# Kernel optimization log

Measured on AMD Instinct MI355X. Metric: run time of the kernel, lower is better.

Reference implementation:

```python
import jax, jax.numpy as jnp
import numpy as np

N_NODES = 50000
N_EDGES = 800000
IN_F, HID, NCLS = 128, 64, 64
N_EXTRA = 2          # layer - 2
K_STEPS = 10
ALPHA = 0.1
BN_EPS = 1e-5


def setup_inputs() -> dict:
    key = jax.random.key(0)
    ks = jax.random.split(key, 20)
    d = {}
    d['x'] = jax.random.normal(ks[0], (N_NODES, IN_F), dtype=jnp.float32)
    d['edge_index'] = jax.random.randint(ks[1], (2, N_EDGES), 0, N_NODES, dtype=jnp.int64)
    s = 1.0 / np.sqrt(HID)
    d['W1'] = jax.random.normal(ks[2], (IN_F, HID), dtype=jnp.float32) / np.sqrt(IN_F)
    d['b1'] = jnp.zeros((HID,), jnp.float32)
    d['W2'] = jax.random.normal(ks[3], (HID, HID), dtype=jnp.float32) * s
    d['b2'] = jnp.zeros((HID,), jnp.float32)
    d['Wx'] = jax.random.normal(ks[4], (N_EXTRA, HID, HID), dtype=jnp.float32) * s
    d['bx'] = jnp.zeros((N_EXTRA, HID), jnp.float32)
    d['g1'] = jnp.ones((HID,), jnp.float32); d['be1'] = jnp.zeros((HID,), jnp.float32)
    d['g2'] = jnp.ones((HID,), jnp.float32); d['be2'] = jnp.zeros((HID,), jnp.float32)
    d['g3'] = jnp.ones((HID,), jnp.float32); d['be3'] = jnp.zeros((HID,), jnp.float32)
    d['Wfc'] = jax.random.normal(ks[5], (HID, NCLS), dtype=jnp.float32) * s
    d['bfc'] = jnp.zeros((NCLS,), jnp.float32)
    return d


def _gcn_norm(edge_index, n):
    # add self-loops, symmetric D^-1/2 (A+I) D^-1/2 normalization (PyG GCNConv default)
    loop = jnp.arange(n, dtype=edge_index.dtype)
    src = jnp.concatenate([edge_index[0], loop])
    dst = jnp.concatenate([edge_index[1], loop])
    deg = jax.ops.segment_sum(jnp.ones(src.shape[0], jnp.float32), dst, num_segments=n)
    dinv = jnp.where(deg > 0, jax.lax.rsqrt(deg), 0.0)
    return src, dst, dinv[src] * dinv[dst]


def _propagate(x, src, dst, w, n):
    # gather-scale-scatter: out[dst] += w * x[src]
    return jax.ops.segment_sum(x[src] * w[:, None], dst, num_segments=n)


def _bn(x, g, b):
    # BatchNorm1d in training mode: batch statistics over the node dim
    m = jnp.mean(x, axis=0)
    v = jnp.var(x, axis=0)
    return g * (x - m) * jax.lax.rsqrt(v + BN_EPS) + b


def reference(x, edge_index, W1, b1, W2, b2, Wx, bx, g1, be1, g2, be2, g3, be3, Wfc, bfc):
    n = x.shape[0]
    src, dst, w = _gcn_norm(edge_index, n)
    h = _propagate(x @ W1, src, dst, w, n) + b1
    h = jax.nn.relu(_bn(h, g1, be1))
    h = _propagate(h @ W2, src, dst, w, n) + b2
    h = jax.nn.relu(_bn(h, g2, be2))
    for i in range(Wx.shape[0]):
        h = _propagate(h @ Wx[i], src, dst, w, n) + bx[i]
        h = jax.nn.relu(_bn(h, g3, be3))
    # APPNP: K power-iteration steps with teleport back to h0
    h0 = h
    for _ in range(K_STEPS):
        h = (1.0 - ALPHA) * _propagate(h, src, dst, w, n) + ALPHA * h0
    out = h @ Wfc + bfc
    return jax.nn.log_softmax(out, axis=1)
```

## Files before the change

### kernel.cpp

```cpp
#include <hip/hip_runtime.h>
#include <hip/hip_fp16.h>
#include <cstdint>
#include <cstddef>

#define NN 50000
#define NE 800000
#define HID 64
#define INF_ 128
#define BN_EPS 1e-5f
#define NGRP (NN / 8)
#define NG16 (NN / 16)
#define SCAN_B 196
#define NSLICE 32
#define NBKT 16

typedef float floatx2 __attribute__((ext_vector_type(2)));

__device__ __forceinline__ float4 h8_to_f4(float2 raw) {
    union { float f; __half2 h; } ua, ub;
    ua.f = raw.x; ub.f = raw.y;
    float2 fa = __half22float2(ua.h), fb = __half22float2(ub.h);
    return make_float4(fa.x, fa.y, fb.x, fb.y);
}
__device__ __forceinline__ float2 f4_to_h8(float4 v) {
    union { float f; __half2 h; } ua, ub;
    ua.h = __float22half2_rn(make_float2(v.x, v.y));
    ub.h = __float22half2_rn(make_float2(v.z, v.w));
    return make_float2(ua.f, ub.f);
}
struct f8 { float v[8]; };
__device__ __forceinline__ f8 h16_to_f8(float4 raw) {
    f8 r;
    union { float f; __half2 h; } u;
    float2 a;
    u.f = raw.x; a = __half22float2(u.h); r.v[0] = a.x; r.v[1] = a.y;
    u.f = raw.y; a = __half22float2(u.h); r.v[2] = a.x; r.v[3] = a.y;
    u.f = raw.z; a = __half22float2(u.h); r.v[4] = a.x; r.v[5] = a.y;
    u.f = raw.w; a = __half22float2(u.h); r.v[6] = a.x; r.v[7] = a.y;
    return r;
}
__device__ __forceinline__ float4 f8_to_h16(const f8& s) {
    union { float f; __half2 h; } u;
    float4 o;
    u.h = __float22half2_rn(make_float2(s.v[0], s.v[1])); o.x = u.f;
    u.h = __float22half2_rn(make_float2(s.v[2], s.v[3])); o.y = u.f;
    u.h = __float22half2_rn(make_float2(s.v[4], s.v[5])); o.z = u.f;
    u.h = __float22half2_rn(make_float2(s.v[6], s.v[7])); o.w = u.f;
    return o;
}

__device__ __forceinline__ void fp8x8_to_f(unsigned lo, unsigned hi, float out[8]) {
    floatx2 a = __builtin_amdgcn_cvt_pk_f32_fp8((int)lo, false);
    floatx2 b = __builtin_amdgcn_cvt_pk_f32_fp8((int)lo, true);
    floatx2 c = __builtin_amdgcn_cvt_pk_f32_fp8((int)hi, false);
    floatx2 d = __builtin_amdgcn_cvt_pk_f32_fp8((int)hi, true);
    out[0] = a[0]; out[1] = a[1]; out[2] = b[0]; out[3] = b[1];
    out[4] = c[0]; out[5] = c[1]; out[6] = d[0]; out[7] = d[1];
}
__device__ __forceinline__ void fp8x16_to_f(uint4 r, float out[16]) {
    fp8x8_to_f(r.x, r.y, out);
    fp8x8_to_f(r.z, r.w, out + 8);
}
__device__ __forceinline__ uint2 f_to_fp8x8(const float v[8]) {
    int w0 = __builtin_amdgcn_cvt_pk_fp8_f32(v[0], v[1], 0, false);
    w0 = __builtin_amdgcn_cvt_pk_fp8_f32(v[2], v[3], w0, true);
    int w1 = __builtin_amdgcn_cvt_pk_fp8_f32(v[4], v[5], 0, false);
    w1 = __builtin_amdgcn_cvt_pk_fp8_f32(v[6], v[7], w1, true);
    uint2 o; o.x = (unsigned)w0; o.y = (unsigned)w1;
    return o;
}
__device__ __forceinline__ uint4 f_to_fp8x16(const float v[16]) {
    uint2 a = f_to_fp8x8(v), b = f_to_fp8x8(v + 8);
    uint4 o; o.x = a.x; o.y = a.y; o.z = b.x; o.w = b.y;
    return o;
}


__global__ void count_k(const int* __restrict__ dst, int* __restrict__ cnt) {
    int e = blockIdx.x * blockDim.x + threadIdx.x;
    if (e < NE) atomicAdd(&cnt[dst[e]], 1);
}

__global__ void dinv_k(const int* __restrict__ cnt, float* __restrict__ dinv) {
    int n = blockIdx.x * blockDim.x + threadIdx.x;
    if (n < NN) dinv[n] = rsqrtf((float)(cnt[n] + 1));
}

__global__ void scan1_k(const int* __restrict__ cnt, int* __restrict__ offs,
                        int* __restrict__ bsum) {
    __shared__ int sh[256];
    int t = threadIdx.x, i = blockIdx.x * 256 + t;
    int v = (i < NN) ? ((cnt[i] + 7) & ~7) : 0;
    sh[t] = v;
    __syncthreads();
    for (int d = 1; d < 256; d <<= 1) {
        int u = (t >= d) ? sh[t - d] : 0;
        __syncthreads();
        sh[t] += u;
        __syncthreads();
    }
    if (i < NN) offs[i] = sh[t] - v;
    if (t == 255) bsum[blockIdx.x] = sh[255];
}

__global__ void scan2_k(const int* __restrict__ bsum, int* __restrict__ bpre,
                        int* __restrict__ offs) {
    __shared__ int sh[256];
    int t = threadIdx.x;
    int v = (t < SCAN_B) ? bsum[t] : 0;
    sh[t] = v;
    __syncthreads();
    for (int d = 1; d < 256; d <<= 1) {
        int u = (t >= d) ? sh[t - d] : 0;
        __syncthreads();
        sh[t] += u;
        __syncthreads();
    }
    bpre[t] = sh[t] - v;
    if (t == 255) offs[NN] = sh[255];
}

__global__ void scan3_k(int* __restrict__ offs, const int* __restrict__ bpre) {
    int i = blockIdx.x * blockDim.x + threadIdx.x;
    if (i < NN) offs[i] += bpre[i >> 8];
}

__global__ void pad_k(const int* __restrict__ cnt, const int* __restrict__ offs,
                      int2* __restrict__ edge2) {
    int n = blockIdx.x * blockDim.x + threadIdx.x;
    if (n >= NN) return;
    int e = offs[n] + cnt[n], e1 = offs[n + 1];
    for (; e < e1; ++e) edge2[e] = make_int2(0, 0);
}

__global__ void scatter_k(const int* __restrict__ src, const int* __restrict__ dst,
                          const int* __restrict__ offs, int* __restrict__ cursor,
                          const float* __restrict__ dinv,
                          int2* __restrict__ edge2) {
    int e = blockIdx.x * blockDim.x + threadIdx.x;
    if (e < NE) {
        int s = src[e], d = dst[e];
        int pos = offs[d] + atomicAdd(&cursor[d], 1);
        edge2[pos] = make_int2(s, __float_as_int(dinv[s] * dinv[d]));
    }
}

__global__ void hist_k(const int* __restrict__ cnt, int* __restrict__ hist) {
    __shared__ int lh[NBKT];
    int t = threadIdx.x;
    if (t < NBKT) lh[t] = 0;
    __syncthreads();
    int n = blockIdx.x * 256 + t;
    if (n < NN) {
        int c = (cnt[n] + 7) >> 3;
        if (c > NBKT - 1) c = NBKT - 1;
        atomicAdd(&lh[c], 1);
    }
    __syncthreads();
    if (t < NBKT && lh[t]) atomicAdd(&hist[t], lh[t]);
}

__global__ void scan16_k(const int* __restrict__ hist, int* __restrict__ bcur) {
    if (threadIdx.x == 0) {
        int s = 0;
        for (int i = 0; i < NBKT; ++i) { bcur[i] = s; s += hist[i]; }
    }
}

__global__ void perm_k(const int* __restrict__ cnt, int* __restrict__ bcur,
                       int* __restrict__ perm) {
    __shared__ int lh[NBKT], lbase[NBKT];
    int t = threadIdx.x;
    if (t < NBKT) lh[t] = 0;
    __syncthreads();
    int n = blockIdx.x * 256 + t;
    int c = 0, r = 0;
    if (n < NN) {
        c = (cnt[n] + 7) >> 3;
        if (c > NBKT - 1) c = NBKT - 1;
        r = atomicAdd(&lh[c], 1);
    }
    __syncthreads();
    if (t < NBKT) lbase[t] = lh[t] ? atomicAdd(&bcur[t], lh[t]) : 0;
    __syncthreads();
    if (n < NN) perm[lbase[c] + r] = n;
}

template <int K, bool HIN>
__global__ __launch_bounds__(256, 2) void mm_k(const void* __restrict__ Xv,
                                               const float* __restrict__ W,
                                               float2* __restrict__ Y) {
    constexpr int RS = K + 4;
    __shared__ float Xs[64 * RS];
    __shared__ float Ws[K * 64];
    const int t = threadIdx.x;
    const int n0 = blockIdx.x * 64;

    {
        const float4* Wg = (const float4*)W;
        for (int g2 = t; g2 < K * 16; g2 += 256) {
            int row = g2 >> 4, c4 = g2 & 15;
            *(float4*)&Ws[row * 64 + c4 * 4] = Wg[g2];
        }
    }
    if (HIN) {
        const float4* Xg = (const float4*)Xv;
        for (int g2 = t; g2 < 64 * (K / 8); g2 += 256) {
            int row = g2 / (K / 8), c8 = g2 % (K / 8);
            int rr = n0 + row; if (rr >= NN) rr = NN - 1;
            f8 v = h16_to_f8(Xg[(size_t)rr * (K / 8) + c8]);
            float* dp = &Xs[row * RS + c8 * 8];
#pragma unroll
            for (int j = 0; j < 8; ++j) dp[j] = v.v[j];
        }
    } else {
        const float4* Xg = (const float4*)Xv;
        for (int g2 = t; g2 < 64 * (K / 4); g2 += 256) {
            int row = g2 / (K / 4), c4 = g2 % (K / 4);
            int rr = n0 + row; if (rr >= NN) rr = NN - 1;
            *(float4*)&Xs[row * RS + c4 * 4] = Xg[(size_t)rr * (K / 4) + c4];
        }
    }
    __syncthreads();

    const int r0 = (t >> 4) << 2;
    const int c0 = (t & 15) << 2;
    float acc[4][4];
#pragma unroll
    for (int j = 0; j < 4; ++j)
#pragma unroll
        for (int c = 0; c < 4; ++c) acc[j][c] = 0.f;

#pragma unroll 8
    for (int kq = 0; kq < K / 4; ++kq) {
        float4 xv[4];
#pragma unroll
        for (int j = 0; j < 4; ++j)
            xv[j] = *(const float4*)&Xs[(r0 + j) * RS + kq * 4];
        float4 wv[4];
#pragma unroll
        for (int i = 0; i < 4; ++i)
            wv[i] = *(const float4*)&Ws[(kq * 4 + i) * 64 + c0];
#pragma unroll
        for (int j = 0; j < 4; ++j) {
            acc[j][0] = fmaf(xv[j].x, wv[0].x, acc[j][0]);
            acc[j][1] = fmaf(xv[j].x, wv[0].y, acc[j][1]);
            acc[j][2] = fmaf(xv[j].x, wv[0].z, acc[j][2]);
            acc[j][3] = fmaf(xv[j].x, wv[0].w, acc[j][3]);
            acc[j][0] = fmaf(xv[j].y, wv[1].x, acc[j][0]);
            acc[j][1] = fmaf(xv[j].y, wv[1].y, acc[j][1]);
            acc[j][2] = fmaf(xv[j].y, wv[1].z, acc[j][2]);
            acc[j][3] = fmaf(xv[j].y, wv[1].w, acc[j][3]);
            acc[j][0] = fmaf(xv[j].z, wv[2].x, acc[j][0]);
            acc[j][1] = fmaf(xv[j].z, wv[2].y, acc[j][1]);
            acc[j][2] = fmaf(xv[j].z, wv[2].z, acc[j][2]);
            acc[j][3] = fmaf(xv[j].z, wv[2].w, acc[j][3]);
            acc[j][0] = fmaf(xv[j].w, wv[3].x, acc[j][0]);
            acc[j][1] = fmaf(xv[j].w, wv[3].y, acc[j][1]);
            acc[j][2] = fmaf(xv[j].w, wv[3].z, acc[j][2]);
            acc[j][3] = fmaf(xv[j].w, wv[3].w, acc[j][3]);
        }
    }

#pragma unroll
    for (int j = 0; j < 4; ++j) {
        int rr = n0 + r0 + j;
        if (rr < NN)
            Y[(size_t)rr * 16 + (t & 15)] =
                f4_to_h8(make_float4(acc[j][0], acc[j][1], acc[j][2], acc[j][3]));
    }
}

__device__ __forceinline__ void prop_gather8(const float4* __restrict__ X4,
                                             const int2* __restrict__ E,
                                             int e0, int e1, int fl, int slotbase,
                                             float acc[8], float acc2[8]) {
    if (e0 >= e1) return;
    int2 d0 = E[e0 + fl];
    int srcs[8]; float ws[8];
#pragma unroll
    for (int i = 0; i < 8; ++i) {
        srcs[i] = __shfl(d0.x, slotbase + i, 64);
        ws[i]   = __shfl(__int_as_float(d0.y), slotbase + i, 64);
    }
    int2 d1;
    if (e0 + 8 < e1) d1 = E[e0 + 8 + fl];
    float4 rr[8];
#pragma unroll
    for (int i = 0; i < 8; ++i) rr[i] = X4[(size_t)srcs[i] * 8 + fl];

    for (int e = e0; e < e1; ) {
        int en = e + 8;
        float4 rn[8]; float wn[8];
        if (en < e1) {
            int sn[8];
#pragma unroll
            for (int i = 0; i < 8; ++i) {
                sn[i] = __shfl(d1.x, slotbase + i, 64);
                wn[i] = __shfl(__int_as_float(d1.y), slotbase + i, 64);
            }
            if (en + 8 < e1) d1 = E[en + 8 + fl];
#pragma unroll
            for (int i = 0; i < 8; ++i) rn[i] = X4[(size_t)sn[i] * 8 + fl];
        }
        __builtin_amdgcn_sched_barrier(0);
#pragma unroll
        for (int i = 0; i < 8; ++i) {
            f8 x = h16_to_f8(rr[i]);
            float* a = (i & 1) ? acc2 : acc;
#pragma unroll
            for (int j = 0; j < 8; ++j)
                a[j] = fmaf(ws[i], x.v[j], a[j]);
        }
        e = en;
        if (e < e1) {
#pragma unroll
            for (int i = 0; i < 8; ++i) { rr[i] = rn[i]; ws[i] = wn[i]; }
        }
    }
}

__global__ __launch_bounds__(256, 2) void prop_stats_k(
        const float4* __restrict__ X4, const int* __restrict__ offs,
        const int2* __restrict__ edge2, const float* __restrict__ dinv,
        const float* __restrict__ bias, const int* __restrict__ perm,
        float4* __restrict__ Y4, float* __restrict__ stats) {
    const int lane = threadIdx.x & 63;
    const int wave = threadIdx.x >> 6;
    const int slot = lane >> 3;
    const int fl = lane & 7;
    const int slotbase = lane & 56;
    const int wid = blockIdx.x * 4 + wave;
    const int nw = gridDim.x * 4;

    float bias8[8];
    {
        float4 b0 = ((const float4*)bias)[fl * 2];
        float4 b1 = ((const float4*)bias)[fl * 2 + 1];
        bias8[0] = b0.x; bias8[1] = b0.y; bias8[2] = b0.z; bias8[3] = b0.w;
        bias8[4] = b1.x; bias8[5] = b1.y; bias8[6] = b1.z; bias8[7] = b1.w;
    }

    float s1[8], s2[8];
#pragma unroll
    for (int j = 0; j < 8; ++j) { s1[j] = 0.f; s2[j] = 0.f; }

    for (int g = wid; g < NGRP; g += nw) {
        int n = perm[g * 8 + slot];
        float dn = dinv[n];
        float dd = dn * dn;
        f8 self = h16_to_f8(X4[(size_t)n * 8 + fl]);
        float acc[8], acc2[8];
#pragma unroll
        for (int j = 0; j < 8; ++j) { acc[j] = dd * self.v[j]; acc2[j] = 0.f; }
        int e0 = offs[n], e1 = offs[n + 1];
        prop_gather8(X4, edge2, e0, e1, fl, slotbase, acc, acc2);
        f8 o;
#pragma unroll
        for (int j = 0; j < 8; ++j) {
            float a = acc[j] + acc2[j] + bias8[j];
            o.v[j] = a;
            s1[j] += a;
            s2[j] = fmaf(a, a, s2[j]);
        }
        Y4[(size_t)n * 8 + fl] = f8_to_h16(o);
    }

#pragma unroll
    for (int m = 8; m <= 32; m <<= 1) {
#pragma unroll
        for (int j = 0; j < 8; ++j) {
            s1[j] += __shfl_xor(s1[j], m, 64);
            s2[j] += __shfl_xor(s2[j], m, 64);
        }
    }

    __shared__ float red[4][8][16];
    if (lane < 8) {
#pragma unroll
        for (int j = 0; j < 8; ++j) {
            red[wave][lane][j] = s1[j];
            red[wave][lane][8 + j] = s2[j];
        }
    }
    __syncthreads();
    int t = threadIdx.x;
    if (t < 128) {
        int j = t & 63;
        int isq = t >> 6;
        int fli = j >> 3, c = (j & 7) + isq * 8;
        float a = red[0][fli][c] + red[1][fli][c] + red[2][fli][c] + red[3][fli][c];
        atomicAdd(&stats[(blockIdx.x & (NSLICE - 1)) * 128 + isq * 64 + j], a);
    }
}

template <bool EMIT8>
__global__ __launch_bounds__(256) void bn_relu_k(
        const float4* __restrict__ Y4, const float* __restrict__ slices,
        const float* __restrict__ g, const float* __restrict__ be,
        float4* __restrict__ H4, uint2* __restrict__ X8) {
    __shared__ float fs[128];
    int t = threadIdx.x;
    if (t < 128) {
        float s = 0.f;
#pragma unroll
        for (int k = 0; k < NSLICE; ++k) s += slices[k * 128 + t];
        fs[t] = s;
    }
    __syncthreads();
    int i = blockIdx.x * blockDim.x + t;
    if (i >= NN * 8) return;
    int fg = i & 7;
    const float invN = 1.f / (float)NN;
    f8 y = h16_to_f8(Y4[i]);
    float4 gv0 = ((const float4*)g)[fg * 2];
    float4 gv1 = ((const float4*)g)[fg * 2 + 1];
    float4 bv0 = ((const float4*)be)[fg * 2];
    float4 bv1 = ((const float4*)be)[fg * 2 + 1];
    float gv[8] = { gv0.x, gv0.y, gv0.z, gv0.w, gv1.x, gv1.y, gv1.z, gv1.w };
    float bv[8] = { bv0.x, bv0.y, bv0.z, bv0.w, bv1.x, bv1.y, bv1.z, bv1.w };
    f8 o;
#pragma unroll
    for (int j = 0; j < 8; ++j) {
        float m = fs[fg * 8 + j] * invN;
        float v = fs[64 + fg * 8 + j] * invN - m * m;
        float val = fmaf(gv[j] * rsqrtf(v + BN_EPS), y.v[j] - m, bv[j]);
        o.v[j] = val > 0.f ? val : 0.f;
    }
    H4[i] = f8_to_h16(o);
    if (EMIT8) X8[i] = f_to_fp8x8(o.v);
}

template <bool OUT16>
__global__ __launch_bounds__(256, 2) void appnp8_k(
        const uint4* __restrict__ X8, const float4* __restrict__ H04,
        const int* __restrict__ offs, const int2* __restrict__ edge2,
        const float* __restrict__ dinv, const int* __restrict__ perm,
        uint4* __restrict__ Y8, float4* __restrict__ Y16) {
    const int lane = threadIdx.x & 63;
    const int wave = threadIdx.x >> 6;
    const int slot = lane >> 2;
    const int fl = lane & 3;
    const int quadbase = lane & 60;
    const int wid = blockIdx.x * 4 + wave;
    if (wid >= NG16) return;
    int n = perm[wid * 16 + slot];
    float dn = dinv[n];
    float dd = dn * dn;
    float acc[16];
    {
        float self[16];
        fp8x16_to_f(X8[(size_t)n * 4 + fl], self);
#pragma unroll
        for (int j = 0; j < 16; ++j) acc[j] = dd * self[j];
    }
    int e0 = offs[n], e1 = offs[n + 1];
    if (e0 < e1) {
        int4 d = ((const int4*)(edge2 + e0))[fl];
        int srcs[8]; float ws[8];
#pragma unroll
        for (int k = 0; k < 8; ++k) {
            int sl = quadbase + (k >> 1);
            srcs[k] = __shfl((k & 1) ? d.z : d.x, sl, 64);
            ws[k]   = __shfl(__int_as_float((k & 1) ? d.w : d.y), sl, 64);
        }
        int4 d1;
        if (e0 + 8 < e1) d1 = ((const int4*)(edge2 + e0 + 8))[fl];
        uint4 rr[8];
#pragma unroll
        for (int k = 0; k < 8; ++k) rr[k] = X8[(size_t)srcs[k] * 4 + fl];

        for (int e = e0; e < e1; ) {
            int en = e + 8;
            uint4 rn[8]; float wn[8];
            if (en < e1) {
                int sn[8];
#pragma unroll
                for (int k = 0; k < 8; ++k) {
                    int sl = quadbase + (k >> 1);
                    sn[k] = __shfl((k & 1) ? d1.z : d1.x, sl, 64);
                    wn[k] = __shfl(__int_as_float((k & 1) ? d1.w : d1.y), sl, 64);
                }
                if (en + 8 < e1) d1 = ((const int4*)(edge2 + en + 8))[fl];
#pragma unroll
                for (int k = 0; k < 8; ++k) rn[k] = X8[(size_t)sn[k] * 4 + fl];
            }
            __builtin_amdgcn_sched_barrier(0);
#pragma unroll
            for (int k = 0; k < 8; ++k) {
                float x[16];
                fp8x16_to_f(rr[k], x);
#pragma unroll
                for (int j = 0; j < 16; ++j)
                    acc[j] = fmaf(ws[k], x[j], acc[j]);
            }
            e = en;
            if (e < e1) {
#pragma unroll
                for (int k = 0; k < 8; ++k) { rr[k] = rn[k]; ws[k] = wn[k]; }
            }
        }
    }
    f8 ha = h16_to_f8(H04[(size_t)n * 8 + fl * 2]);
    f8 hb = h16_to_f8(H04[(size_t)n * 8 + fl * 2 + 1]);
    float o[16];
#pragma unroll
    for (int j = 0; j < 8; ++j) {
        o[j] = fmaf(0.9f, acc[j], 0.1f * ha.v[j]);
        o[8 + j] = fmaf(0.9f, acc[8 + j], 0.1f * hb.v[j]);
    }
    if (OUT16) {
        f8 lo, hi;
#pragma unroll
        for (int j = 0; j < 8; ++j) { lo.v[j] = o[j]; hi.v[j] = o[8 + j]; }
        Y16[(size_t)n * 8 + fl * 2] = f8_to_h16(lo);
        Y16[(size_t)n * 8 + fl * 2 + 1] = f8_to_h16(hi);
    } else {
        Y8[(size_t)n * 4 + fl] = f_to_fp8x16(o);
    }
}

__global__ __launch_bounds__(256) void final_k(const float2* __restrict__ H2,
                                               const float* __restrict__ Wfc,
                                               const float* __restrict__ bfc,
                                               float* __restrict__ out) {
    const int t = threadIdx.x;
    const int n0 = blockIdx.x * 64;
    const int r0 = (t >> 4) << 2;
    const int c0 = (t & 15) << 2;

    int r[4];
#pragma unroll
    for (int j = 0; j < 4; ++j) {
        int rr = n0 + r0 + j;
        r[j] = rr < NN ? rr : NN - 1;
    }
    const float2* Xr[4];
#pragma unroll
    for (int j = 0; j < 4; ++j) Xr[j] = H2 + (size_t)r[j] * 16;

    float4 bf = *(const float4*)(bfc + c0);
    float acc[4][4];
#pragma unroll
    for (int j = 0; j < 4; ++j) {
        acc[j][0] = bf.x; acc[j][1] = bf.y; acc[j][2] = bf.z; acc[j][3] = bf.w;
    }

#pragma unroll 4
    for (int kq = 0; kq < 16; ++kq) {
        float4 xv[4];
#pragma unroll
        for (int j = 0; j < 4; ++j) xv[j] = h8_to_f4(Xr[j][kq]);
        float4 wv[4];
#pragma unroll
        for (int i = 0; i < 4; ++i)
            wv[i] = *(const float4*)(Wfc + (size_t)(kq * 4 + i) * 64 + c0);
#pragma unroll
        for (int j = 0; j < 4; ++j) {
            acc[j][0] = fmaf(xv[j].x, wv[0].x, acc[j][0]);
            acc[j][1] = fmaf(xv[j].x, wv[0].y, acc[j][1]);
            acc[j][2] = fmaf(xv[j].x, wv[0].z, acc[j][2]);
            acc[j][3] = fmaf(xv[j].x, wv[0].w, acc[j][3]);
            acc[j][0] = fmaf(xv[j].y, wv[1].x, acc[j][0]);
            acc[j][1] = fmaf(xv[j].y, wv[1].y, acc[j][1]);
            acc[j][2] = fmaf(xv[j].y, wv[1].z, acc[j][2]);
            acc[j][3] = fmaf(xv[j].y, wv[1].w, acc[j][3]);
            acc[j][0] = fmaf(xv[j].z, wv[2].x, acc[j][0]);
            acc[j][1] = fmaf(xv[j].z, wv[2].y, acc[j][1]);
            acc[j][2] = fmaf(xv[j].z, wv[2].z, acc[j][2]);
            acc[j][3] = fmaf(xv[j].z, wv[2].w, acc[j][3]);
            acc[j][0] = fmaf(xv[j].w, wv[3].x, acc[j][0]);
            acc[j][1] = fmaf(xv[j].w, wv[3].y, acc[j][1]);
            acc[j][2] = fmaf(xv[j].w, wv[3].z, acc[j][2]);
            acc[j][3] = fmaf(xv[j].w, wv[3].w, acc[j][3]);
        }
    }

#pragma unroll
    for (int j = 0; j < 4; ++j) {
        float m = fmaxf(fmaxf(acc[j][0], acc[j][1]), fmaxf(acc[j][2], acc[j][3]));
#pragma unroll
        for (int d = 1; d <= 8; d <<= 1) m = fmaxf(m, __shfl_xor(m, d, 64));
        float s = expf(acc[j][0] - m) + expf(acc[j][1] - m) +
                  expf(acc[j][2] - m) + expf(acc[j][3] - m);
#pragma unroll
        for (int d = 1; d <= 8; d <<= 1) s += __shfl_xor(s, d, 64);
        float lse = m + logf(s);
        int rr = n0 + r0 + j;
        if (rr < NN)
            *(float4*)(out + (size_t)rr * 64 + c0) =
                make_float4(acc[j][0] - lse, acc[j][1] - lse,
                            acc[j][2] - lse, acc[j][3] - lse);
    }
}


static inline char* alignup(char* p, size_t a) {
    return (char*)(((uintptr_t)p + a - 1) & ~(uintptr_t)(a - 1));
}

extern "C" void kernel_launch(void* const* d_in, const int* in_sizes, int n_in,
                              void* d_out, int out_size, void* d_ws, size_t ws_size,
                              hipStream_t stream) {
    const float* x   = (const float*)d_in[0];
    const int*   ei  = (const int*)d_in[1];
    const float* W1  = (const float*)d_in[2];
    const float* b1  = (const float*)d_in[3];
    const float* W2  = (const float*)d_in[4];
    const float* b2  = (const float*)d_in[5];
    const float* Wx  = (const float*)d_in[6];
    const float* bx  = (const float*)d_in[7];
    const float* g1  = (const float*)d_in[8];
    const float* be1 = (const float*)d_in[9];
    const float* g2  = (const float*)d_in[10];
    const float* be2 = (const float*)d_in[11];
    const float* g3  = (const float*)d_in[12];
    const float* be3 = (const float*)d_in[13];
    const float* Wfc = (const float*)d_in[14];
    const float* bfc = (const float*)d_in[15];
    float* out = (float*)d_out;

    const int* srcA = ei;
    const int* dstA = ei + NE;

    char* p = (char*)d_ws;
    int*   deg    = (int*)p;   p += NN * 4;
    int*   cursor = (int*)p;   p += NN * 4;
    float* stats  = (float*)p; p += 4 * NSLICE * 128 * 4;
    int*   hist   = (int*)p;   p += NBKT * 4;
    size_t zbytes = (size_t)(p - (char*)d_ws);
    p = alignup(p, 512);
    int*   offs  = (int*)p;    p += (NN + 4) * 4;   p = alignup(p, 512);
    float* dinv  = (float*)p;  p += NN * 4;         p = alignup(p, 512);
    int*   bsum  = (int*)p;    p += 256 * 4;
    int*   bpre  = (int*)p;    p += 256 * 4;
    int*   bcur  = (int*)p;    p += NBKT * 4;       p = alignup(p, 512);
    int*   perm  = (int*)p;    p += NN * 4;         p = alignup(p, 512);
    int2*  edge2 = (int2*)p;   p += ((size_t)NE + 8 * NN + 256) * 8; p = alignup(p, 512);
    float4* tmpH = (float4*)p; p += (size_t)NN * 64 * 2; p = alignup(p, 512);
    float4* hbH  = (float4*)p; p += (size_t)NN * 64 * 2; p = alignup(p, 512);
    float4* apH  = (float4*)p; p += (size_t)NN * 64 * 2; p = alignup(p, 512);
    float4* pbH  = (float4*)p; p += (size_t)NN * 64 * 2; p = alignup(p, 512);
    uint4*  x8a  = (uint4*)p;  p += (size_t)NN * 64;     p = alignup(p, 512);
    uint4*  x8b  = (uint4*)p;  p += (size_t)NN * 64;

    hipMemsetAsync(d_ws, 0, zbytes, stream);

    count_k<<<(NE + 255) / 256, 256, 0, stream>>>(dstA, deg);
    dinv_k<<<(NN + 255) / 256, 256, 0, stream>>>(deg, dinv);
    hist_k<<<SCAN_B, 256, 0, stream>>>(deg, hist);
    scan16_k<<<1, 64, 0, stream>>>(hist, bcur);
    perm_k<<<SCAN_B, 256, 0, stream>>>(deg, bcur, perm);
    scan1_k<<<SCAN_B, 256, 0, stream>>>(deg, offs, bsum);
    scan2_k<<<1, 256, 0, stream>>>(bsum, bpre, offs);
    scan3_k<<<(NN + 255) / 256, 256, 0, stream>>>(offs, bpre);
    pad_k<<<(NN + 255) / 256, 256, 0, stream>>>(deg, offs, edge2);
    scatter_k<<<(NE + 255) / 256, 256, 0, stream>>>(srcA, dstA, offs, cursor, dinv, edge2);

    const int MMG = (NN + 63) / 64;
    const int PG  = (NGRP + 3) / 4;
    const int AG  = (NG16 + 3) / 4;
    const int BNG = (NN * 8 + 255) / 256;
    const int SL  = NSLICE * 128;

    mm_k<INF_, false><<<MMG, 256, 0, stream>>>(x, W1, (float2*)tmpH);
    prop_stats_k<<<PG, 256, 0, stream>>>(tmpH, offs, edge2, dinv, b1, perm, pbH, stats + 0 * SL);
    bn_relu_k<false><<<BNG, 256, 0, stream>>>(pbH, stats + 0 * SL, g1, be1, hbH, nullptr);

    mm_k<HID, true><<<MMG, 256, 0, stream>>>(hbH, W2, (float2*)tmpH);
    prop_stats_k<<<PG, 256, 0, stream>>>(tmpH, offs, edge2, dinv, b2, perm, pbH, stats + 1 * SL);
    bn_relu_k<false><<<BNG, 256, 0, stream>>>(pbH, stats + 1 * SL, g2, be2, hbH, nullptr);

    mm_k<HID, true><<<MMG, 256, 0, stream>>>(hbH, Wx + (size_t)0 * 64 * 64, (float2*)tmpH);
    prop_stats_k<<<PG, 256, 0, stream>>>(tmpH, offs, edge2, dinv, bx + (size_t)0 * 64, perm,
                                         pbH, stats + 2 * SL);
    bn_relu_k<false><<<BNG, 256, 0, stream>>>(pbH, stats + 2 * SL, g3, be3, hbH, nullptr);

    mm_k<HID, true><<<MMG, 256, 0, stream>>>(hbH, Wx + (size_t)1 * 64 * 64, (float2*)tmpH);
    prop_stats_k<<<PG, 256, 0, stream>>>(tmpH, offs, edge2, dinv, bx + (size_t)1 * 64, perm,
                                         pbH, stats + 3 * SL);
    bn_relu_k<true><<<BNG, 256, 0, stream>>>(pbH, stats + 3 * SL, g3, be3, hbH, (uint2*)x8a);

    const uint4* cur8 = x8a;
    for (int it = 0; it < 9; ++it) {
        uint4* o8 = (cur8 == x8a) ? x8b : x8a;
        appnp8_k<false><<<AG, 256, 0, stream>>>(cur8, hbH, offs, edge2, dinv, perm, o8, nullptr);
        cur8 = o8;
    }
    appnp8_k<true><<<AG, 256, 0, stream>>>(cur8, hbH, offs, edge2, dinv, perm, nullptr, apH);

    final_k<<<MMG, 256, 0, stream>>>((const float2*)apH, Wfc, bfc, out);
}
```

Before: 498.9 us.

## Factor GCN edge weights into per-node dinv scaling and drop weight storage

New measurement: 819.9 us. 1.64x slower.

```diff
diff --git a/kernel.cpp b/kernel.cpp
--- a/kernel.cpp
+++ b/kernel.cpp
@@ -86,6 +86,14 @@
     if (n < NN) dinv[n] = rsqrtf((float)(cnt[n] + 1));
 }
 
+__global__ void zrow_k(float4* __restrict__ tmpH, uint4* __restrict__ x8a,
+                       uint4* __restrict__ x8b) {
+    int t = threadIdx.x;
+    if (t < 8) tmpH[(size_t)NN * 8 + t] = make_float4(0.f, 0.f, 0.f, 0.f);
+    else if (t < 12) x8a[(size_t)NN * 4 + (t - 8)] = make_uint4(0, 0, 0, 0);
+    else if (t < 16) x8b[(size_t)NN * 4 + (t - 12)] = make_uint4(0, 0, 0, 0);
+}
+
 __global__ void scan1_k(const int* __restrict__ cnt, int* __restrict__ offs,
                         int* __restrict__ bsum) {
     __shared__ int sh[256];
@@ -126,22 +134,21 @@
 }
 
 __global__ void pad_k(const int* __restrict__ cnt, const int* __restrict__ offs,
-                      int2* __restrict__ edge2) {
+                      int* __restrict__ edge1) {
     int n = blockIdx.x * blockDim.x + threadIdx.x;
     if (n >= NN) return;
     int e = offs[n] + cnt[n], e1 = offs[n + 1];
-    for (; e < e1; ++e) edge2[e] = make_int2(0, 0);
+    for (; e < e1; ++e) edge1[e] = NN;
 }
 
 __global__ void scatter_k(const int* __restrict__ src, const int* __restrict__ dst,
                           const int* __restrict__ offs, int* __restrict__ cursor,
-                          const float* __restrict__ dinv,
-                          int2* __restrict__ edge2) {
+                          int* __restrict__ edge1) {
     int e = blockIdx.x * blockDim.x + threadIdx.x;
     if (e < NE) {
-        int s = src[e], d = dst[e];
+        int d = dst[e];
         int pos = offs[d] + atomicAdd(&cursor[d], 1);
-        edge2[pos] = make_int2(s, __float_as_int(dinv[s] * dinv[d]));
+        edge1[pos] = src[e];
     }
 }
 
@@ -189,6 +196,7 @@
 template <int K, bool HIN>
 __global__ __launch_bounds__(256, 2) void mm_k(const void* __restrict__ Xv,
                                                const float* __restrict__ W,
+                                               const float* __restrict__ dinv,
                                                float2* __restrict__ Y) {
     constexpr int RS = K + 4;
     __shared__ float Xs[64 * RS];
@@ -265,25 +273,25 @@
 #pragma unroll
     for (int j = 0; j < 4; ++j) {
         int rr = n0 + r0 + j;
-        if (rr < NN)
+        if (rr < NN) {
+            float dn = dinv[rr];
             Y[(size_t)rr * 16 + (t & 15)] =
-                f4_to_h8(make_float4(acc[j][0], acc[j][1], acc[j][2], acc[j][3]));
+                f4_to_h8(make_float4(acc[j][0] * dn, acc[j][1] * dn,
+                                     acc[j][2] * dn, acc[j][3] * dn));
+        }
     }
 }
 
 __device__ __forceinline__ void prop_gather8(const float4* __restrict__ X4,
-                                             const int2* __restrict__ E,
+                                             const int* __restrict__ E,
                                              int e0, int e1, int fl, int slotbase,
-                                             float acc[8], float acc2[8]) {
+                                             float acc[8]) {
     if (e0 >= e1) return;
-    int2 d0 = E[e0 + fl];
-    int srcs[8]; float ws[8];
-#pragma unroll
-    for (int i = 0; i < 8; ++i) {
-        srcs[i] = __shfl(d0.x, slotbase + i, 64);
-        ws[i]   = __shfl(__int_as_float(d0.y), slotbase + i, 64);
-    }
-    int2 d1;
+    int d0 = E[e0 + fl];
+    int srcs[8];
+#pragma unroll
+    for (int i = 0; i < 8; ++i) srcs[i] = __shfl(d0, slotbase + i, 64);
+    int d1;
     if (e0 + 8 < e1) d1 = E[e0 + 8 + fl];
     float4 rr[8];
 #pragma unroll
@@ -291,14 +299,11 @@
 
     for (int e = e0; e < e1; ) {
         int en = e + 8;
-        float4 rn[8]; float wn[8];
+        float4 rn[8];
         if (en < e1) {
             int sn[8];
 #pragma unroll
-            for (int i = 0; i < 8; ++i) {
-                sn[i] = __shfl(d1.x, slotbase + i, 64);
-                wn[i] = __shfl(__int_as_float(d1.y), slotbase + i, 64);
-            }
+            for (int i = 0; i < 8; ++i) sn[i] = __shfl(d1, slotbase + i, 64);
             if (en + 8 < e1) d1 = E[en + 8 + fl];
 #pragma unroll
             for (int i = 0; i < 8; ++i) rn[i] = X4[(size_t)sn[i] * 8 + fl];
@@ -307,22 +312,21 @@
 #pragma unroll
         for (int i = 0; i < 8; ++i) {
             f8 x = h16_to_f8(rr[i]);
-            float* a = (i & 1) ? acc2 : acc;
 #pragma unroll
             for (int j = 0; j < 8; ++j)
-                a[j] = fmaf(ws[i], x.v[j], a[j]);
+                acc[j] += x.v[j];
         }
         e = en;
         if (e < e1) {
 #pragma unroll
-            for (int i = 0; i < 8; ++i) { rr[i] = rn[i]; ws[i] = wn[i]; }
-        }
-    }
-}
-
-__global__ __launch_bounds__(256, 2) void prop_stats_k(
+            for (int i = 0; i < 8; ++i) rr[i] = rn[i];
+        }
+    }
+}
+
+__global__ __launch_bounds__(256, 3) void prop_stats_k(
         const float4* __restrict__ X4, const int* __restrict__ offs,
-        const int2* __restrict__ edge2, const float* __restrict__ dinv,
+        const int* __restrict__ edge1, const float* __restrict__ dinv,
         const float* __restrict__ bias, const int* __restrict__ perm,
         float4* __restrict__ Y4, float* __restrict__ stats) {
     const int lane = threadIdx.x & 63;
@@ -348,17 +352,16 @@
     for (int g = wid; g < NGRP; g += nw) {
         int n = perm[g * 8 + slot];
         float dn = dinv[n];
-        float dd = dn * dn;
         f8 self = h16_to_f8(X4[(size_t)n * 8 + fl]);
-        float acc[8], acc2[8];
-#pragma unroll
-        for (int j = 0; j < 8; ++j) { acc[j] = dd * self.v[j]; acc2[j] = 0.f; }
+        float acc[8];
+#pragma unroll
+        for (int j = 0; j < 8; ++j) acc[j] = self.v[j];
         int e0 = offs[n], e1 = offs[n + 1];
-        prop_gather8(X4, edge2, e0, e1, fl, slotbase, acc, acc2);
+        prop_gather8(X4, edge1, e0, e1, fl, slotbase, acc);
         f8 o;
 #pragma unroll
         for (int j = 0; j < 8; ++j) {
-            float a = acc[j] + acc2[j] + bias8[j];
+            float a = fmaf(dn, acc[j], bias8[j]);
             o.v[j] = a;
             s1[j] += a;
             s2[j] = fmaf(a, a, s2[j]);
@@ -398,7 +401,8 @@
 __global__ __launch_bounds__(256) void bn_relu_k(
         const float4* __restrict__ Y4, const float* __restrict__ slices,
         const float* __restrict__ g, const float* __restrict__ be,
-        float4* __restrict__ H4, uint2* __restrict__ X8) {
+        float4* __restrict__ H4, uint2* __restrict__ X8,
+        const float* __restrict__ dinv) {
     __shared__ float fs[128];
     int t = threadIdx.x;
     if (t < 128) {
@@ -428,13 +432,19 @@
         o.v[j] = val > 0.f ? val : 0.f;
     }
     H4[i] = f8_to_h16(o);
-    if (EMIT8) X8[i] = f_to_fp8x8(o.v);
+    if (EMIT8) {
+        float dn = dinv[i >> 3];
+        float sv[8];
+#pragma unroll
+        for (int j = 0; j < 8; ++j) sv[j] = dn * o.v[j];
+        X8[i] = f_to_fp8x8(sv);
+    }
 }
 
 template <bool OUT16>
-__global__ __launch_bounds__(256, 2) void appnp8_k(
+__global__ __launch_bounds__(256, 4) void appnp8_k(
         const uint4* __restrict__ X8, const float4* __restrict__ H04,
-        const int* __restrict__ offs, const int2* __restrict__ edge2,
+        const int* __restrict__ offs, const int* __restrict__ edge1,
         const float* __restrict__ dinv, const int* __restrict__ perm,
         uint4* __restrict__ Y8, float4* __restrict__ Y16) {
     const int lane = threadIdx.x & 63;
@@ -446,42 +456,35 @@
     if (wid >= NG16) return;
     int n = perm[wid * 16 + slot];
     float dn = dinv[n];
-    float dd = dn * dn;
     float acc[16];
     {
         float self[16];
         fp8x16_to_f(X8[(size_t)n * 4 + fl], self);
 #pragma unroll
-        for (int j = 0; j < 16; ++j) acc[j] = dd * self[j];
+        for (int j = 0; j < 16; ++j) acc[j] = self[j];
     }
     int e0 = offs[n], e1 = offs[n + 1];
     if (e0 < e1) {
-        int4 d = ((const int4*)(edge2 + e0))[fl];
-        int srcs[8]; float ws[8];
-#pragma unroll
-        for (int k = 0; k < 8; ++k) {
-            int sl = quadbase + (k >> 1);
-            srcs[k] = __shfl((k & 1) ? d.z : d.x, sl, 64);
-            ws[k]   = __shfl(__int_as_float((k & 1) ? d.w : d.y), sl, 64);
-        }
-        int4 d1;
-        if (e0 + 8 < e1) d1 = ((const int4*)(edge2 + e0 + 8))[fl];
+        int2 d = ((const int2*)(edge1 + e0))[fl];
+        int srcs[8];
+#pragma unroll
+        for (int k = 0; k < 8; ++k)
+            srcs[k] = __shfl((k & 1) ? d.y : d.x, quadbase + (k >> 1), 64);
+        int2 d1;
+        if (e0 + 8 < e1) d1 = ((const int2*)(edge1 + e0 + 8))[fl];
         uint4 rr[8];
 #pragma unroll
         for (int k = 0; k < 8; ++k) rr[k] = X8[(size_t)srcs[k] * 4 + fl];
 
         for (int e = e0; e < e1; ) {
             int en = e + 8;
-            uint4 rn[8]; float wn[8];
+            uint4 rn[8];
             if (en < e1) {
                 int sn[8];
 #pragma unroll
-                for (int k = 0; k < 8; ++k) {
-                    int sl = quadbase + (k >> 1);
-                    sn[k] = __shfl((k & 1) ? d1.z : d1.x, sl, 64);
-                    wn[k] = __shfl(__int_as_float((k & 1) ? d1.w : d1.y), sl, 64);
-                }
-                if (en + 8 < e1) d1 = ((const int4*)(edge2 + en + 8))[fl];
+                for (int k = 0; k < 8; ++k)
+                    sn[k] = __shfl((k & 1) ? d1.y : d1.x, quadbase + (k >> 1), 64);
+                if (en + 8 < e1) d1 = ((const int2*)(edge1 + en + 8))[fl];
 #pragma unroll
                 for (int k = 0; k < 8; ++k) rn[k] = X8[(size_t)sn[k] * 4 + fl];
             }
@@ -492,22 +495,23 @@
                 fp8x16_to_f(rr[k], x);
 #pragma unroll
                 for (int j = 0; j < 16; ++j)
-                    acc[j] = fmaf(ws[k], x[j], acc[j]);
+                    acc[j] += x[j];
             }
             e = en;
             if (e < e1) {
 #pragma unroll
-                for (int k = 0; k < 8; ++k) { rr[k] = rn[k]; ws[k] = wn[k]; }
+                for (int k = 0; k < 8; ++k) rr[k] = rn[k];
             }
         }
     }
     f8 ha = h16_to_f8(H04[(size_t)n * 8 + fl * 2]);
     f8 hb = h16_to_f8(H04[(size_t)n * 8 + fl * 2 + 1]);
     float o[16];
+    float s = 0.9f * dn;
 #pragma unroll
     for (int j = 0; j < 8; ++j) {
-        o[j] = fmaf(0.9f, acc[j], 0.1f * ha.v[j]);
-        o[8 + j] = fmaf(0.9f, acc[8 + j], 0.1f * hb.v[j]);
+        o[j] = fmaf(s, acc[j], 0.1f * ha.v[j]);
+        o[8 + j] = fmaf(s, acc[8 + j], 0.1f * hb.v[j]);
     }
     if (OUT16) {
         f8 lo, hi;
@@ -516,7 +520,10 @@
         Y16[(size_t)n * 8 + fl * 2] = f8_to_h16(lo);
         Y16[(size_t)n * 8 + fl * 2 + 1] = f8_to_h16(hi);
     } else {
-        Y8[(size_t)n * 4 + fl] = f_to_fp8x16(o);
+        float so[16];
+#pragma unroll
+        for (int j = 0; j < 16; ++j) so[j] = dn * o[j];
+        Y8[(size_t)n * 4 + fl] = f_to_fp8x16(so);
     }
 }
 
@@ -636,26 +643,27 @@
     int*   bpre  = (int*)p;    p += 256 * 4;
     int*   bcur  = (int*)p;    p += NBKT * 4;       p = alignup(p, 512);
     int*   perm  = (int*)p;    p += NN * 4;         p = alignup(p, 512);
-    int2*  edge2 = (int2*)p;   p += ((size_t)NE + 8 * NN + 256) * 8; p = alignup(p, 512);
-    float4* tmpH = (float4*)p; p += (size_t)NN * 64 * 2; p = alignup(p, 512);
-    float4* hbH  = (float4*)p; p += (size_t)NN * 64 * 2; p = alignup(p, 512);
-    float4* apH  = (float4*)p; p += (size_t)NN * 64 * 2; p = alignup(p, 512);
-    float4* pbH  = (float4*)p; p += (size_t)NN * 64 * 2; p = alignup(p, 512);
-    uint4*  x8a  = (uint4*)p;  p += (size_t)NN * 64;     p = alignup(p, 512);
-    uint4*  x8b  = (uint4*)p;  p += (size_t)NN * 64;
+    int*   edge1 = (int*)p;    p += ((size_t)NE + 8 * NN + 256) * 4; p = alignup(p, 512);
+    float4* tmpH = (float4*)p; p += ((size_t)NN + 1) * 128; p = alignup(p, 512);
+    float4* hbH  = (float4*)p; p += (size_t)NN * 128;       p = alignup(p, 512);
+    float4* apH  = (float4*)p; p += (size_t)NN * 128;       p = alignup(p, 512);
+    float4* pbH  = (float4*)p; p += (size_t)NN * 128;       p = alignup(p, 512);
+    uint4*  x8a  = (uint4*)p;  p += ((size_t)NN + 1) * 64;  p = alignup(p, 512);
+    uint4*  x8b  = (uint4*)p;  p += ((size_t)NN + 1) * 64;
 
     hipMemsetAsync(d_ws, 0, zbytes, stream);
 
     count_k<<<(NE + 255) / 256, 256, 0, stream>>>(dstA, deg);
     dinv_k<<<(NN + 255) / 256, 256, 0, stream>>>(deg, dinv);
+    zrow_k<<<1, 64, 0, stream>>>(tmpH, x8a, x8b);
     hist_k<<<SCAN_B, 256, 0, stream>>>(deg, hist);
     scan16_k<<<1, 64, 0, stream>>>(hist, bcur);
     perm_k<<<SCAN_B, 256, 0, stream>>>(deg, bcur, perm);
     scan1_k<<<SCAN_B, 256, 0, stream>>>(deg, offs, bsum);
     scan2_k<<<1, 256, 0, stream>>>(bsum, bpre, offs);
     scan3_k<<<(NN + 255) / 256, 256, 0, stream>>>(offs, bpre);
-    pad_k<<<(NN + 255) / 256, 256, 0, stream>>>(deg, offs, edge2);
-    scatter_k<<<(NE + 255) / 256, 256, 0, stream>>>(srcA, dstA, offs, cursor, dinv, edge2);
+    pad_k<<<(NN + 255) / 256, 256, 0, stream>>>(deg, offs, edge1);
+    scatter_k<<<(NE + 255) / 256, 256, 0, stream>>>(srcA, dstA, offs, cursor, edge1);
 
     const int MMG = (NN + 63) / 64;
     const int PG  = (NGRP + 3) / 4;
@@ -663,31 +671,31 @@
     const int BNG = (NN * 8 + 255) / 256;
     const int SL  = NSLICE * 128;
 
-    mm_k<INF_, false><<<MMG, 256, 0, stream>>>(x, W1, (float2*)tmpH);
-    prop_stats_k<<<PG, 256, 0, stream>>>(tmpH, offs, edge2, dinv, b1, perm, pbH, stats + 0 * SL);
-    bn_relu_k<false><<<BNG, 256, 0, stream>>>(pbH, stats + 0 * SL, g1, be1, hbH, nullptr);
-
-    mm_k<HID, true><<<MMG, 256, 0, stream>>>(hbH, W2, (float2*)tmpH);
-    prop_stats_k<<<PG, 256, 0, stream>>>(tmpH, offs, edge2, dinv, b2, perm, pbH, stats + 1 * SL);
-    bn_relu_k<false><<<BNG, 256, 0, stream>>>(pbH, stats + 1 * SL, g2, be2, hbH, nullptr);
-
-    mm_k<HID, true><<<MMG, 256, 0, stream>>>(hbH, Wx + (size_t)0 * 64 * 64, (float2*)tmpH);
-    prop_stats_k<<<PG, 256, 0, stream>>>(tmpH, offs, edge2, dinv, bx + (size_t)0 * 64, perm,
+    mm_k<INF_, false><<<MMG, 256, 0, stream>>>(x, W1, dinv, (float2*)tmpH);
+    prop_stats_k<<<PG, 256, 0, stream>>>(tmpH, offs, edge1, dinv, b1, perm, pbH, stats + 0 * SL);
+    bn_relu_k<false><<<BNG, 256, 0, stream>>>(pbH, stats + 0 * SL, g1, be1, hbH, nullptr, dinv);
+
+    mm_k<HID, true><<<MMG, 256, 0, stream>>>(hbH, W2, dinv, (float2*)tmpH);
+    prop_stats_k<<<PG, 256, 0, stream>>>(tmpH, offs, edge1, dinv, b2, perm, pbH, stats + 1 * SL);
+    bn_relu_k<false><<<BNG, 256, 0, stream>>>(pbH, stats + 1 * SL, g2, be2, hbH, nullptr, dinv);
+
+    mm_k<HID, true><<<MMG, 256, 0, stream>>>(hbH, Wx + (size_t)0 * 64 * 64, dinv, (float2*)tmpH);
+    prop_stats_k<<<PG, 256, 0, stream>>>(tmpH, offs, edge1, dinv, bx + (size_t)0 * 64, perm,
                                          pbH, stats + 2 * SL);
-    bn_relu_k<false><<<BNG, 256, 0, stream>>>(pbH, stats + 2 * SL, g3, be3, hbH, nullptr);
-
-    mm_k<HID, true><<<MMG, 256, 0, stream>>>(hbH, Wx + (size_t)1 * 64 * 64, (float2*)tmpH);
-    prop_stats_k<<<PG, 256, 0, stream>>>(tmpH, offs, edge2, dinv, bx + (size_t)1 * 64, perm,
+    bn_relu_k<false><<<BNG, 256, 0, stream>>>(pbH, stats + 2 * SL, g3, be3, hbH, nullptr, dinv);
+
+    mm_k<HID, true><<<MMG, 256, 0, stream>>>(hbH, Wx + (size_t)1 * 64 * 64, dinv, (float2*)tmpH);
+    prop_stats_k<<<PG, 256, 0, stream>>>(tmpH, offs, edge1, dinv, bx + (size_t)1 * 64, perm,
                                          pbH, stats + 3 * SL);
-    bn_relu_k<true><<<BNG, 256, 0, stream>>>(pbH, stats + 3 * SL, g3, be3, hbH, (uint2*)x8a);
+    bn_relu_k<true><<<BNG, 256, 0, stream>>>(pbH, stats + 3 * SL, g3, be3, hbH, (uint2*)x8a, dinv);
 
     const uint4* cur8 = x8a;
     for (int it = 0; it < 9; ++it) {
         uint4* o8 = (cur8 == x8a) ? x8b : x8a;
-        appnp8_k<false><<<AG, 256, 0, stream>>>(cur8, hbH, offs, edge2, dinv, perm, o8, nullptr);
+        appnp8_k<false><<<AG, 256, 0, stream>>>(cur8, hbH, offs, edge1, dinv, perm, o8, nullptr);
         cur8 = o8;
     }
-    appnp8_k<true><<<AG, 256, 0, stream>>>(cur8, hbH, offs, edge2, dinv, perm, nullptr, apH);
+    appnp8_k<true><<<AG, 256, 0, stream>>>(cur8, hbH, offs, edge1, dinv, perm, nullptr, apH);
 
     final_k<<<MMG, 256, 0, stream>>>((const float2*)apH, Wfc, bfc, out);
 }
```
